# Kernel tuning notes

Measured on AMD Instinct MI355X. Metric: run time of the kernel, lower is better.

Reference implementation:

```python
import jax, jax.numpy as jnp
import numpy as np

H = 1024
B = 8
T = 2048

def setup_inputs() -> dict:
    key = jax.random.key(0)
    ks = jax.random.split(key, 12)
    s = 1.0 / np.sqrt(H)
    return {
        "x": jax.random.normal(ks[0], (B, T, H), dtype=jnp.float32),
        "time_decay": jax.random.normal(ks[1], (H,), dtype=jnp.float32) * 0.1,
        "time_first": jax.random.normal(ks[2], (H,), dtype=jnp.float32) * 0.1,
        "time_mix_key": jax.random.uniform(ks[3], (1, 1, H), dtype=jnp.float32),
        "time_mix_value": jax.random.uniform(ks[4], (1, 1, H), dtype=jnp.float32),
        "time_mix_receptance": jax.random.uniform(ks[5], (1, 1, H), dtype=jnp.float32),
        "Wk": jax.random.normal(ks[6], (H, H), dtype=jnp.float32) * s,
        "Wv": jax.random.normal(ks[7], (H, H), dtype=jnp.float32) * s,
        "Wr": jax.random.normal(ks[8], (H, H), dtype=jnp.float32) * s,
        "Wo": jax.random.normal(ks[9], (H, H), dtype=jnp.float32) * s,
        "bo": jax.random.normal(ks[10], (H,), dtype=jnp.float32) * 0.01,
    }

def reference(x, time_decay, time_first, time_mix_key, time_mix_value,
              time_mix_receptance, Wk, Wv, Wr, Wo, bo):
    # time shift: shifted[:, t] = x[:, t-1], shifted[:, 0] = 0
    shifted = jnp.pad(x, ((0, 0), (1, 0), (0, 0)))[:, :-1]
    k_in = x * time_mix_key + shifted * (1.0 - time_mix_key)
    v_in = x * time_mix_value + shifted * (1.0 - time_mix_value)
    r_in = x * time_mix_receptance + shifted * (1.0 - time_mix_receptance)
    k = jnp.einsum('bth,oh->bto', k_in, Wk)
    v = jnp.einsum('bth,oh->bto', v_in, Wv)
    r = jax.nn.sigmoid(jnp.einsum('bth,oh->bto', r_in, Wr))

    td = jnp.exp(-jnp.exp(time_decay))  # (H,)

    def step(carry, kv):
        num, den = carry            # (B, H) each
        k_t, v_t = kv               # (B, H) each
        e = jnp.exp(time_first + k_t)
        out_t = (num + e * v_t) / (den + e)
        ek = jnp.exp(k_t)
        return (td * num + ek * v_t, td * den + ek), out_t

    init = (jnp.zeros((x.shape[0], x.shape[2]), x.dtype),
            jnp.zeros((x.shape[0], x.shape[2]), x.dtype))
    # scan over time: (T, B, H)
    _, wkv = jax.lax.scan(step, init, (k.transpose(1, 0, 2), v.transpose(1, 0, 2)))
    wkv = wkv.transpose(1, 0, 2)    # (B, T, H)

    return jnp.einsum('bth,oh->bto', r * wkv, Wo) + bo
```

## Files before the change

kernel.cpp:

```cpp
#include <hip/hip_runtime.h>
#include <hip/hip_bf16.h>
#include <cstdint>
#include <cstddef>

#define HH 1024
#define BB 8
#define TT 2048
#define MM (BB*TT)
#define CC 256
#define LL (TT/CC)

typedef __attribute__((ext_vector_type(8))) short bf16x8;
typedef __attribute__((ext_vector_type(8))) unsigned short u16x8;
typedef __attribute__((ext_vector_type(4))) float f32x4;

__device__ __forceinline__ unsigned short f2bf(float f) {
  union { float f; unsigned u; } v; v.f = f;
  return (unsigned short)((v.u + 0x7fffu + ((v.u >> 16) & 1u)) >> 16);
}
__device__ __forceinline__ float bf2f(unsigned short s) {
  union { float f; unsigned u; } v; v.u = ((unsigned)s) << 16;
  return v.f;
}

__device__ __forceinline__ void load_lds16(const void* g, void* l) {
  __builtin_amdgcn_global_load_lds((const __attribute__((address_space(1))) void*)g,
                                   (__attribute__((address_space(3))) void*)l,
                                   16, 0, 0);
}

__global__ __launch_bounds__(256) void conv_w(const float* __restrict__ Wk,
    const float* __restrict__ Wv, const float* __restrict__ Wr,
    const float* __restrict__ Wo, unsigned short* __restrict__ dst) {
  const int i = (blockIdx.x * 256 + threadIdx.x) * 4;
  const float* src = blockIdx.y == 0 ? Wk : blockIdx.y == 1 ? Wv : blockIdx.y == 2 ? Wr : Wo;
  const float4 v = *(const float4*)(src + i);
  ushort4 o; o.x = f2bf(v.x); o.y = f2bf(v.y); o.z = f2bf(v.z); o.w = f2bf(v.w);
  *(ushort4*)(dst + (size_t)blockIdx.y * HH * HH + i) = o;
}

__global__ __launch_bounds__(256) void mix_kernel(const float* __restrict__ x,
    const float* __restrict__ tmk, const float* __restrict__ tmv, const float* __restrict__ tmr,
    unsigned short* __restrict__ kin, unsigned short* __restrict__ vin,
    unsigned short* __restrict__ rin) {
  const int gid = blockIdx.x * 256 + threadIdx.x;
  const size_t e0 = (size_t)gid * 4;
  const int h = (int)(e0 & (HH - 1));
  const int t = (int)((e0 >> 10) & (TT - 1));
  const float4 xv = *(const float4*)(x + e0);
  float4 sv = make_float4(0.f, 0.f, 0.f, 0.f);
  if (t != 0) sv = *(const float4*)(x + e0 - HH);
  const float4 k4 = *(const float4*)(tmk + h);
  const float4 v4 = *(const float4*)(tmv + h);
  const float4 r4 = *(const float4*)(tmr + h);
  ushort4 ko, vo, ro;
  ko.x = f2bf(sv.x + k4.x * (xv.x - sv.x)); ko.y = f2bf(sv.y + k4.y * (xv.y - sv.y));
  ko.z = f2bf(sv.z + k4.z * (xv.z - sv.z)); ko.w = f2bf(sv.w + k4.w * (xv.w - sv.w));
  vo.x = f2bf(sv.x + v4.x * (xv.x - sv.x)); vo.y = f2bf(sv.y + v4.y * (xv.y - sv.y));
  vo.z = f2bf(sv.z + v4.z * (xv.z - sv.z)); vo.w = f2bf(sv.w + v4.w * (xv.w - sv.w));
  ro.x = f2bf(sv.x + r4.x * (xv.x - sv.x)); ro.y = f2bf(sv.y + r4.y * (xv.y - sv.y));
  ro.z = f2bf(sv.z + r4.z * (xv.z - sv.z)); ro.w = f2bf(sv.w + r4.w * (xv.w - sv.w));
  *(ushort4*)(kin + e0) = ko;
  *(ushort4*)(vin + e0) = vo;
  *(ushort4*)(rin + e0) = ro;
}


#define BAR()   do { asm volatile("" ::: "memory"); __builtin_amdgcn_s_barrier(); \
                     asm volatile("" ::: "memory"); } while (0)
#define SB0()   __builtin_amdgcn_sched_barrier(0)
#define VM4()   asm volatile("s_waitcnt vmcnt(4)" ::: "memory")
#define VM0()   asm volatile("s_waitcnt vmcnt(0)" ::: "memory")

__device__ __forceinline__ void stA(const unsigned short* __restrict__ Ag, int m0, int kt,
                                    unsigned short* buf, int h, int w, int rl, int scol) {
#pragma unroll
  for (int l = 0; l < 2; ++l) {
    const int row = l * 128 + h * 64 + w * 8;
    load_lds16(Ag + (size_t)(m0 + row + rl) * HH + kt + scol, buf + row * 64);
  }
}
__device__ __forceinline__ void stB(const unsigned short* __restrict__ Bg, int n0, int kt,
                                    unsigned short* buf, int h, int w, int rl, int scol) {
#pragma unroll
  for (int l = 0; l < 2; ++l) {
    const int row = (2 * (l * 2 + (w >> 2)) + h) * 32 + (w & 3) * 8;
    load_lds16(Bg + (size_t)(n0 + row + rl) * HH + kt + scol, buf + row * 64);
  }
}

template<int MH, int FH>
__device__ __forceinline__ void rdA_h(const unsigned short* buf, bf16x8 (&af)[4][2],
                                      int wm, int l15, int kq, int swz) {
#pragma unroll
  for (int fm = FH * 2; fm < FH * 2 + 2; ++fm)
#pragma unroll
    for (int kk = 0; kk < 2; ++kk)
      af[fm][kk] = *(const bf16x8*)(buf + (wm * 128 + MH * 64 + fm * 16 + l15) * 64
                                        + ((kk * 32 + kq * 8) ^ swz));
}
template<int NH>
__device__ __forceinline__ void rdB(const unsigned short* buf, bf16x8 (&bfr)[2][2][2],
                                    int wn, int l15, int kq, int swz) {
#pragma unroll
  for (int fn = 0; fn < 2; ++fn)
#pragma unroll
    for (int kk = 0; kk < 2; ++kk)
      bfr[NH][fn][kk] = *(const bf16x8*)(buf + (wn * 64 + NH * 32 + fn * 16 + l15) * 64
                                             + ((kk * 32 + kq * 8) ^ swz));
}
template<int MH, int NH, int FH>
__device__ __forceinline__ void mfma8(f32x4 (&acc)[8][4], const bf16x8 (&af)[4][2],
                                      const bf16x8 (&bfr)[2][2][2]) {
#pragma unroll
  for (int kk = 0; kk < 2; ++kk)
#pragma unroll
    for (int fm = FH * 2; fm < FH * 2 + 2; ++fm)
#pragma unroll
      for (int fn = 0; fn < 2; ++fn)
        acc[MH * 4 + fm][NH * 2 + fn] = __builtin_amdgcn_mfma_f32_16x16x32_bf16(
            bfr[NH][fn][kk], af[fm][kk], acc[MH * 4 + fm][NH * 2 + fn], 0, 0, 0);
}

__device__ __forceinline__ void gemm256(const unsigned short* __restrict__ Ag,
                                        const unsigned short* __restrict__ Bg,
                                        const int m0, const int n0,
                                        unsigned short* As, unsigned short* Bs,
                                        f32x4 (&acc)[8][4]) {
  const int tid = threadIdx.x;
  const int lane = tid & 63;
  const int w = tid >> 6;
  const int wm = w >> 2, wn = w & 3;
  const int l15 = lane & 15, kq = lane >> 4;
  const int swz = (l15 & 7) << 3;
  const int rl = lane >> 3;
  const int scol = ((lane & 7) ^ rl) * 8;
  unsigned short* const A0 = As;
  unsigned short* const A1 = As + 256 * 64;
  unsigned short* const B0 = Bs;
  unsigned short* const B1 = Bs + 256 * 64;
  bf16x8 af[4][2], bfr[2][2][2];

  stA(Ag, m0, 0, A0, 0, w, rl, scol);
  stB(Bg, n0, 0, B0, 0, w, rl, scol);
  stB(Bg, n0, 0, B0, 1, w, rl, scol);
  stA(Ag, m0, 0, A0, 1, w, rl, scol);
  stA(Ag, m0, 64, A1, 0, w, rl, scol);
  stB(Bg, n0, 64, B1, 0, w, rl, scol);
  VM4();
  BAR();

#pragma unroll 1
  for (int i = 0; i < 8; ++i) {
    const int t1  = ((2 * i + 1) * 64) & (HH - 1);
    const int tn0 = ((2 * i + 2) * 64) & (HH - 1);
    const int tn1 = ((2 * i + 3) * 64) & (HH - 1);

    rdA_h<0, 0>(A0, af, wm, l15, kq, swz); SB0();
    rdB<0>(B0, bfr, wn, l15, kq, swz);     SB0();
    rdA_h<0, 1>(A0, af, wm, l15, kq, swz); SB0();
    rdB<1>(B0, bfr, wn, l15, kq, swz);
    stB(Bg, n0, t1, B1, 1, w, rl, scol);
    stA(Ag, m0, t1, A1, 1, w, rl, scol);
    BAR(); SB0();
    __builtin_amdgcn_s_setprio(1);
    mfma8<0, 0, 0>(acc, af, bfr); SB0();
    mfma8<0, 0, 1>(acc, af, bfr); SB0();
    mfma8<0, 1, 0>(acc, af, bfr);
    mfma8<0, 1, 1>(acc, af, bfr);
    __builtin_amdgcn_s_setprio(0);
    BAR();
    rdA_h<1, 0>(A0, af, wm, l15, kq, swz); SB0();
    rdA_h<1, 1>(A0, af, wm, l15, kq, swz);
    stA(Ag, m0, tn0, A0, 0, w, rl, scol);
    stB(Bg, n0, tn0, B0, 0, w, rl, scol);
    BAR(); SB0();
    __builtin_amdgcn_s_setprio(1);
    mfma8<1, 0, 0>(acc, af, bfr);
    mfma8<1, 1, 0>(acc, af, bfr); SB0();
    mfma8<1, 0, 1>(acc, af, bfr);
    mfma8<1, 1, 1>(acc, af, bfr);
    __builtin_amdgcn_s_setprio(0);
    VM4();
    BAR();
    rdA_h<0, 0>(A1, af, wm, l15, kq, swz); SB0();
    rdB<0>(B1, bfr, wn, l15, kq, swz);     SB0();
    rdA_h<0, 1>(A1, af, wm, l15, kq, swz); SB0();
    rdB<1>(B1, bfr, wn, l15, kq, swz);
    stB(Bg, n0, tn0, B0, 1, w, rl, scol);
    stA(Ag, m0, tn0, A0, 1, w, rl, scol);
    BAR(); SB0();
    __builtin_amdgcn_s_setprio(1);
    mfma8<0, 0, 0>(acc, af, bfr); SB0();
    mfma8<0, 0, 1>(acc, af, bfr); SB0();
    mfma8<0, 1, 0>(acc, af, bfr);
    mfma8<0, 1, 1>(acc, af, bfr);
    __builtin_amdgcn_s_setprio(0);
    BAR();
    rdA_h<1, 0>(A1, af, wm, l15, kq, swz); SB0();
    rdA_h<1, 1>(A1, af, wm, l15, kq, swz);
    stA(Ag, m0, tn1, A1, 0, w, rl, scol);
    stB(Bg, n0, tn1, B1, 0, w, rl, scol);
    BAR(); SB0();
    __builtin_amdgcn_s_setprio(1);
    mfma8<1, 0, 0>(acc, af, bfr);
    mfma8<1, 1, 0>(acc, af, bfr); SB0();
    mfma8<1, 0, 1>(acc, af, bfr);
    mfma8<1, 1, 1>(acc, af, bfr);
    __builtin_amdgcn_s_setprio(0);
    VM4();
    BAR();
  }
  VM0();
}

__device__ __forceinline__ void swizzle_mn256(int x, int& m0, int& n0) {
  const int wg = (x & 7) * 32 + (x >> 3);
  m0 = (wg >> 2) * 256;
  n0 = (wg & 3) * 256;
}

__global__ __launch_bounds__(512, 2) void gemm_kvr(const unsigned short* __restrict__ kin,
    const unsigned short* __restrict__ vin, const unsigned short* __restrict__ rin,
    const unsigned short* __restrict__ Wbf,
    unsigned short* __restrict__ kb, unsigned short* __restrict__ vb,
    unsigned short* __restrict__ rb) {
  __shared__ unsigned short As[2 * 256 * 64];
  __shared__ unsigned short Bs[2 * 256 * 64];
  const int z = blockIdx.y;
  const unsigned short* Ag = z == 0 ? kin : (z == 1 ? vin : rin);
  const unsigned short* Bg = Wbf + (size_t)z * HH * HH;
  unsigned short* Cg = z == 0 ? kb : (z == 1 ? vb : rb);
  int m0, n0; swizzle_mn256(blockIdx.x, m0, n0);
  f32x4 acc[8][4] = {};
  gemm256(Ag, Bg, m0, n0, As, Bs, acc);
  const int lane = threadIdx.x & 63, w = threadIdx.x >> 6;
  const int wm = w >> 2, wn = w & 3, l15 = lane & 15, lq = lane >> 4;
  const bool sig = (z == 2);
#pragma unroll
  for (int fm = 0; fm < 8; ++fm) {
    const size_t mrow = (size_t)(m0 + wm * 128 + fm * 16 + l15) * HH;
#pragma unroll
    for (int fn = 0; fn < 4; ++fn) {
      const int ncol = n0 + wn * 64 + fn * 16 + lq * 4;
      float v0 = acc[fm][fn][0], v1 = acc[fm][fn][1];
      float v2 = acc[fm][fn][2], v3 = acc[fm][fn][3];
      if (sig) {
        v0 = 1.0f / (1.0f + __expf(-v0)); v1 = 1.0f / (1.0f + __expf(-v1));
        v2 = 1.0f / (1.0f + __expf(-v2)); v3 = 1.0f / (1.0f + __expf(-v3));
      }
      ushort4 o; o.x = f2bf(v0); o.y = f2bf(v1); o.z = f2bf(v2); o.w = f2bf(v3);
      *(ushort4*)(Cg + mrow + ncol) = o;
    }
  }
}

__global__ __launch_bounds__(512, 2) void gemm_o(const unsigned short* __restrict__ Ag,
    const unsigned short* __restrict__ Bg, const float* __restrict__ bias,
    float* __restrict__ C) {
  __shared__ unsigned short As[2 * 256 * 64];
  __shared__ unsigned short Bs[2 * 256 * 64];
  int m0, n0; swizzle_mn256(blockIdx.x, m0, n0);
  f32x4 acc[8][4] = {};
  gemm256(Ag, Bg, m0, n0, As, Bs, acc);
  const int lane = threadIdx.x & 63, w = threadIdx.x >> 6;
  const int wm = w >> 2, wn = w & 3, l15 = lane & 15, lq = lane >> 4;
#pragma unroll
  for (int fm = 0; fm < 8; ++fm) {
    const size_t mrow = (size_t)(m0 + wm * 128 + fm * 16 + l15) * HH;
#pragma unroll
    for (int fn = 0; fn < 4; ++fn) {
      const int ncol = n0 + wn * 64 + fn * 16 + lq * 4;
      const float4 bv = *(const float4*)(bias + ncol);
      float4 ov;
      ov.x = acc[fm][fn][0] + bv.x; ov.y = acc[fm][fn][1] + bv.y;
      ov.z = acc[fm][fn][2] + bv.z; ov.w = acc[fm][fn][3] + bv.w;
      *(float4*)(C + mrow + ncol) = ov;
    }
  }
}

__global__ __launch_bounds__(256) void wkv_part(const unsigned short* __restrict__ k,
    const unsigned short* __restrict__ v, const float* __restrict__ tdec,
    float* __restrict__ pnum, float* __restrict__ pden) {
  const int gid = blockIdx.x * 256 + threadIdx.x;
  const int h0 = (gid & 127) * 8;
  const int b = (gid >> 7) & (BB - 1);
  const int c = gid >> 10;
  float td[8], num[8], den[8];
#pragma unroll
  for (int j = 0; j < 8; ++j) {
    td[j] = __expf(-__expf(tdec[h0 + j]));
    num[j] = 0.f; den[j] = 0.f;
  }
  size_t idx = (size_t)b * TT * HH + (size_t)(c * LL) * HH + h0;
#pragma unroll
  for (int i = 0; i < LL; ++i, idx += HH) {
    const u16x8 k8 = *(const u16x8*)(k + idx);
    const u16x8 v8 = *(const u16x8*)(v + idx);
#pragma unroll
    for (int j = 0; j < 8; ++j) {
      const float ek = __expf(bf2f(k8[j]));
      num[j] = td[j] * num[j] + ek * bf2f(v8[j]);
      den[j] = td[j] * den[j] + ek;
    }
  }
  const size_t o = (size_t)c * (BB * HH) + b * HH + h0;
#pragma unroll
  for (int j = 0; j < 8; ++j) { pnum[o + j] = num[j]; pden[o + j] = den[j]; }
}

__global__ __launch_bounds__(256) void wkv_scan(const float* __restrict__ tdec,
    float* __restrict__ pnum, float* __restrict__ pden) {
  const int bh = blockIdx.x * 256 + threadIdx.x;
  const int h = bh & (HH - 1);
  const float ed = __expf(tdec[h]);
  const float tdL = __expf(-ed * (float)LL);
  float num = 0.f, den = 0.f;
#pragma unroll 8
  for (int c = 0; c < CC; ++c) {
    const size_t o = (size_t)c * (BB * HH) + bh;
    const float tn = pnum[o], td_ = pden[o];
    pnum[o] = num; pden[o] = den;
    num = tdL * num + tn;
    den = tdL * den + td_;
  }
}

__global__ __launch_bounds__(256) void wkv_final(const unsigned short* __restrict__ k,
    const unsigned short* __restrict__ v, const unsigned short* __restrict__ r,
    const float* __restrict__ tdec, const float* __restrict__ tfst,
    const float* __restrict__ pnum, const float* __restrict__ pden,
    unsigned short* __restrict__ rwkv) {
  const int gid = blockIdx.x * 256 + threadIdx.x;
  const int h0 = (gid & 127) * 8;
  const int b = (gid >> 7) & (BB - 1);
  const int c = gid >> 10;
  float td[8], etf[8], num[8], den[8];
  const size_t o = (size_t)c * (BB * HH) + b * HH + h0;
#pragma unroll
  for (int j = 0; j < 8; ++j) {
    td[j] = __expf(-__expf(tdec[h0 + j]));
    etf[j] = __expf(tfst[h0 + j]);
    num[j] = pnum[o + j]; den[j] = pden[o + j];
  }
  size_t idx = (size_t)b * TT * HH + (size_t)(c * LL) * HH + h0;
#pragma unroll
  for (int i = 0; i < LL; ++i, idx += HH) {
    const u16x8 k8 = *(const u16x8*)(k + idx);
    const u16x8 v8 = *(const u16x8*)(v + idx);
    const u16x8 r8 = *(const u16x8*)(r + idx);
    u16x8 o8;
#pragma unroll
    for (int j = 0; j < 8; ++j) {
      const float ek = __expf(bf2f(k8[j]));
      const float vt = bf2f(v8[j]);
      const float rt = bf2f(r8[j]);
      const float e = ek * etf[j];
      const float inv = __builtin_amdgcn_rcpf(den[j] + e);
      const float outv = (num[j] + e * vt) * inv;
      num[j] = td[j] * num[j] + ek * vt;
      den[j] = td[j] * den[j] + ek;
      o8[j] = f2bf(outv * rt);
    }
    *(u16x8*)(rwkv + idx) = o8;
  }
}

extern "C" void kernel_launch(void* const* d_in, const int* in_sizes, int n_in,
                              void* d_out, int out_size, void* d_ws, size_t ws_size,
                              hipStream_t stream) {
  (void)in_sizes; (void)n_in; (void)out_size; (void)ws_size;
  const float* x    = (const float*)d_in[0];
  const float* tdec = (const float*)d_in[1];
  const float* tfst = (const float*)d_in[2];
  const float* tmk  = (const float*)d_in[3];
  const float* tmv  = (const float*)d_in[4];
  const float* tmr  = (const float*)d_in[5];
  const float* Wk   = (const float*)d_in[6];
  const float* Wv   = (const float*)d_in[7];
  const float* Wr   = (const float*)d_in[8];
  const float* Wo   = (const float*)d_in[9];
  const float* bo   = (const float*)d_in[10];
  float* out = (float*)d_out;

  char* ws = (char*)d_ws;
  const size_t MiB = (size_t)1 << 20;
  unsigned short* Wbf = (unsigned short*)(ws);
  unsigned short* kin = (unsigned short*)(ws + 8 * MiB);
  unsigned short* vin = (unsigned short*)(ws + 40 * MiB);
  unsigned short* rin = (unsigned short*)(ws + 72 * MiB);
  unsigned short* rb  = (unsigned short*)(ws + 104 * MiB);
  unsigned short* kb = (unsigned short*)out;
  unsigned short* vb = kb + (size_t)MM * HH;
  unsigned short* rwkv = kin;
  float* pnum = (float*)(ws + 40 * MiB);
  float* pden = (float*)(ws + 48 * MiB);

  hipLaunchKernelGGL(conv_w, dim3(1024, 4), dim3(256), 0, stream, Wk, Wv, Wr, Wo, Wbf);
  hipLaunchKernelGGL(mix_kernel, dim3(16384), dim3(256), 0, stream,
                     x, tmk, tmv, tmr, kin, vin, rin);
  hipLaunchKernelGGL(gemm_kvr, dim3(256, 3), dim3(512), 0, stream,
                     kin, vin, rin, Wbf, kb, vb, rb);
  hipLaunchKernelGGL(wkv_part, dim3(1024), dim3(256), 0, stream,
                     kb, vb, tdec, pnum, pden);
  hipLaunchKernelGGL(wkv_scan, dim3(32), dim3(256), 0, stream,
                     tdec, pnum, pden);
  hipLaunchKernelGGL(wkv_final, dim3(1024), dim3(256), 0, stream,
                     kb, vb, rb, tdec, tfst, pnum, pden, rwkv);
  hipLaunchKernelGGL(gemm_o, dim3(256), dim3(512), 0, stream,
                     rwkv, Wbf + (size_t)3 * HH * HH, bo, out);
}
```

Measured before the change: 374.1 us.

## Restructure GEMM main loop with register double-buffering and halve WKV chunk count

The GEMM inner loop now reads A fragments into two alternating register sets and loads all B fragments at once, so the next half-tile's LDS reads overlap the current MFMA block. Sched barriers are removed and the loop waits for all global loads instead of leaving four in flight. Separately, the WKV scan uses 128 chunks instead of 256, giving longer sequential runs per thread, fewer partial states and half the grid, with reduced unrolling. This trades more register pressure and less parallelism in the WKV kernels for fewer barriers and less partial-state traffic.

Measured after the change: 431.9 us. +15.5%, slower.

```diff
diff --git a/kernel.cpp b/kernel.cpp
--- a/kernel.cpp
+++ b/kernel.cpp
@@ -7,7 +7,7 @@
 #define BB 8
 #define TT 2048
 #define MM (BB*TT)
-#define CC 256
+#define CC 128
 #define LL (TT/CC)
 
 typedef __attribute__((ext_vector_type(8))) short bf16x8;
@@ -68,9 +68,10 @@
 
 #define BAR()   do { asm volatile("" ::: "memory"); __builtin_amdgcn_s_barrier(); \
                      asm volatile("" ::: "memory"); } while (0)
-#define SB0()   __builtin_amdgcn_sched_barrier(0)
 #define VM4()   asm volatile("s_waitcnt vmcnt(4)" ::: "memory")
 #define VM0()   asm volatile("s_waitcnt vmcnt(0)" ::: "memory")
+#define PRIO1() __builtin_amdgcn_s_setprio(1)
+#define PRIO0() __builtin_amdgcn_s_setprio(0)
 
 __device__ __forceinline__ void stA(const unsigned short* __restrict__ Ag, int m0, int kt,
                                     unsigned short* buf, int h, int w, int rl, int scol) {
@@ -89,37 +90,40 @@
   }
 }
 
-template<int MH, int FH>
-__device__ __forceinline__ void rdA_h(const unsigned short* buf, bf16x8 (&af)[4][2],
-                                      int wm, int l15, int kq, int swz) {
-#pragma unroll
-  for (int fm = FH * 2; fm < FH * 2 + 2; ++fm)
+template<int MH>
+__device__ __forceinline__ void rdA(const unsigned short* buf, bf16x8 (&af)[4][2],
+                                    int wm, int l15, int kq, int swz) {
+#pragma unroll
+  for (int fm = 0; fm < 4; ++fm)
 #pragma unroll
     for (int kk = 0; kk < 2; ++kk)
       af[fm][kk] = *(const bf16x8*)(buf + (wm * 128 + MH * 64 + fm * 16 + l15) * 64
                                         + ((kk * 32 + kq * 8) ^ swz));
 }
-template<int NH>
-__device__ __forceinline__ void rdB(const unsigned short* buf, bf16x8 (&bfr)[2][2][2],
-                                    int wn, int l15, int kq, int swz) {
-#pragma unroll
-  for (int fn = 0; fn < 2; ++fn)
-#pragma unroll
-    for (int kk = 0; kk < 2; ++kk)
-      bfr[NH][fn][kk] = *(const bf16x8*)(buf + (wn * 64 + NH * 32 + fn * 16 + l15) * 64
-                                             + ((kk * 32 + kq * 8) ^ swz));
-}
-template<int MH, int NH, int FH>
-__device__ __forceinline__ void mfma8(f32x4 (&acc)[8][4], const bf16x8 (&af)[4][2],
-                                      const bf16x8 (&bfr)[2][2][2]) {
-#pragma unroll
-  for (int kk = 0; kk < 2; ++kk)
-#pragma unroll
-    for (int fm = FH * 2; fm < FH * 2 + 2; ++fm)
-#pragma unroll
-      for (int fn = 0; fn < 2; ++fn)
-        acc[MH * 4 + fm][NH * 2 + fn] = __builtin_amdgcn_mfma_f32_16x16x32_bf16(
-            bfr[NH][fn][kk], af[fm][kk], acc[MH * 4 + fm][NH * 2 + fn], 0, 0, 0);
+__device__ __forceinline__ void rdBall(const unsigned short* buf, bf16x8 (&bfr)[2][2][2],
+                                       int wn, int l15, int kq, int swz) {
+#pragma unroll
+  for (int nh = 0; nh < 2; ++nh)
+#pragma unroll
+    for (int fn = 0; fn < 2; ++fn)
+#pragma unroll
+      for (int kk = 0; kk < 2; ++kk)
+        bfr[nh][fn][kk] = *(const bf16x8*)(buf + (wn * 64 + nh * 32 + fn * 16 + l15) * 64
+                                               + ((kk * 32 + kq * 8) ^ swz));
+}
+template<int MH>
+__device__ __forceinline__ void mfma32(f32x4 (&acc)[8][4], const bf16x8 (&af)[4][2],
+                                       const bf16x8 (&bfr)[2][2][2]) {
+#pragma unroll
+  for (int nh = 0; nh < 2; ++nh)
+#pragma unroll
+    for (int fn = 0; fn < 2; ++fn)
+#pragma unroll
+      for (int kk = 0; kk < 2; ++kk)
+#pragma unroll
+        for (int fm = 0; fm < 4; ++fm)
+          acc[MH * 4 + fm][nh * 2 + fn] = __builtin_amdgcn_mfma_f32_16x16x32_bf16(
+              bfr[nh][fn][kk], af[fm][kk], acc[MH * 4 + fm][nh * 2 + fn], 0, 0, 0);
 }
 
 __device__ __forceinline__ void gemm256(const unsigned short* __restrict__ Ag,
@@ -139,7 +143,7 @@
   unsigned short* const A1 = As + 256 * 64;
   unsigned short* const B0 = Bs;
   unsigned short* const B1 = Bs + 256 * 64;
-  bf16x8 af[4][2], bfr[2][2][2];
+  bf16x8 afA[4][2], afB[4][2], bfr[2][2][2];
 
   stA(Ag, m0, 0, A0, 0, w, rl, scol);
   stB(Bg, n0, 0, B0, 0, w, rl, scol);
@@ -149,6 +153,8 @@
   stB(Bg, n0, 64, B1, 0, w, rl, scol);
   VM4();
   BAR();
+  rdA<0>(A0, afA, wm, l15, kq, swz);
+  rdBall(B0, bfr, wn, l15, kq, swz);
 
 #pragma unroll 1
   for (int i = 0; i < 8; ++i) {
@@ -156,60 +162,33 @@
     const int tn0 = ((2 * i + 2) * 64) & (HH - 1);
     const int tn1 = ((2 * i + 3) * 64) & (HH - 1);
 
-    rdA_h<0, 0>(A0, af, wm, l15, kq, swz); SB0();
-    rdB<0>(B0, bfr, wn, l15, kq, swz);     SB0();
-    rdA_h<0, 1>(A0, af, wm, l15, kq, swz); SB0();
-    rdB<1>(B0, bfr, wn, l15, kq, swz);
+    BAR();
     stB(Bg, n0, t1, B1, 1, w, rl, scol);
     stA(Ag, m0, t1, A1, 1, w, rl, scol);
-    BAR(); SB0();
-    __builtin_amdgcn_s_setprio(1);
-    mfma8<0, 0, 0>(acc, af, bfr); SB0();
-    mfma8<0, 0, 1>(acc, af, bfr); SB0();
-    mfma8<0, 1, 0>(acc, af, bfr);
-    mfma8<0, 1, 1>(acc, af, bfr);
-    __builtin_amdgcn_s_setprio(0);
+    rdA<1>(A0, afB, wm, l15, kq, swz);
+    PRIO1(); mfma32<0>(acc, afA, bfr); PRIO0();
+
+    VM0();
     BAR();
-    rdA_h<1, 0>(A0, af, wm, l15, kq, swz); SB0();
-    rdA_h<1, 1>(A0, af, wm, l15, kq, swz);
     stA(Ag, m0, tn0, A0, 0, w, rl, scol);
     stB(Bg, n0, tn0, B0, 0, w, rl, scol);
-    BAR(); SB0();
-    __builtin_amdgcn_s_setprio(1);
-    mfma8<1, 0, 0>(acc, af, bfr);
-    mfma8<1, 1, 0>(acc, af, bfr); SB0();
-    mfma8<1, 0, 1>(acc, af, bfr);
-    mfma8<1, 1, 1>(acc, af, bfr);
-    __builtin_amdgcn_s_setprio(0);
-    VM4();
+    rdA<0>(A1, afA, wm, l15, kq, swz);
+    PRIO1(); mfma32<1>(acc, afB, bfr); PRIO0();
+    rdBall(B1, bfr, wn, l15, kq, swz);
+
     BAR();
-    rdA_h<0, 0>(A1, af, wm, l15, kq, swz); SB0();
-    rdB<0>(B1, bfr, wn, l15, kq, swz);     SB0();
-    rdA_h<0, 1>(A1, af, wm, l15, kq, swz); SB0();
-    rdB<1>(B1, bfr, wn, l15, kq, swz);
     stB(Bg, n0, tn0, B0, 1, w, rl, scol);
     stA(Ag, m0, tn0, A0, 1, w, rl, scol);
-    BAR(); SB0();
-    __builtin_amdgcn_s_setprio(1);
-    mfma8<0, 0, 0>(acc, af, bfr); SB0();
-    mfma8<0, 0, 1>(acc, af, bfr); SB0();
-    mfma8<0, 1, 0>(acc, af, bfr);
-    mfma8<0, 1, 1>(acc, af, bfr);
-    __builtin_amdgcn_s_setprio(0);
+    rdA<1>(A1, afB, wm, l15, kq, swz);
+    PRIO1(); mfma32<0>(acc, afA, bfr); PRIO0();
+
+    VM0();
     BAR();
-    rdA_h<1, 0>(A1, af, wm, l15, kq, swz); SB0();
-    rdA_h<1, 1>(A1, af, wm, l15, kq, swz);
     stA(Ag, m0, tn1, A1, 0, w, rl, scol);
     stB(Bg, n0, tn1, B1, 0, w, rl, scol);
-    BAR(); SB0();
-    __builtin_amdgcn_s_setprio(1);
-    mfma8<1, 0, 0>(acc, af, bfr);
-    mfma8<1, 1, 0>(acc, af, bfr); SB0();
-    mfma8<1, 0, 1>(acc, af, bfr);
-    mfma8<1, 1, 1>(acc, af, bfr);
-    __builtin_amdgcn_s_setprio(0);
-    VM4();
-    BAR();
+    rdA<0>(A0, afA, wm, l15, kq, swz);
+    PRIO1(); mfma32<1>(acc, afB, bfr); PRIO0();
+    rdBall(B0, bfr, wn, l15, kq, swz);
   }
   VM0();
 }
@@ -294,7 +273,7 @@
     num[j] = 0.f; den[j] = 0.f;
   }
   size_t idx = (size_t)b * TT * HH + (size_t)(c * LL) * HH + h0;
-#pragma unroll
+#pragma unroll 4
   for (int i = 0; i < LL; ++i, idx += HH) {
     const u16x8 k8 = *(const u16x8*)(k + idx);
     const u16x8 v8 = *(const u16x8*)(v + idx);
@@ -345,7 +324,7 @@
     num[j] = pnum[o + j]; den[j] = pden[o + j];
   }
   size_t idx = (size_t)b * TT * HH + (size_t)(c * LL) * HH + h0;
-#pragma unroll
+#pragma unroll 2
   for (int i = 0; i < LL; ++i, idx += HH) {
     const u16x8 k8 = *(const u16x8*)(k + idx);
     const u16x8 v8 = *(const u16x8*)(v + idx);
@@ -395,18 +374,18 @@
   unsigned short* vb = kb + (size_t)MM * HH;
   unsigned short* rwkv = kin;
   float* pnum = (float*)(ws + 40 * MiB);
-  float* pden = (float*)(ws + 48 * MiB);
+  float* pden = (float*)(ws + 44 * MiB);
 
   hipLaunchKernelGGL(conv_w, dim3(1024, 4), dim3(256), 0, stream, Wk, Wv, Wr, Wo, Wbf);
   hipLaunchKernelGGL(mix_kernel, dim3(16384), dim3(256), 0, stream,
                      x, tmk, tmv, tmr, kin, vin, rin);
   hipLaunchKernelGGL(gemm_kvr, dim3(256, 3), dim3(512), 0, stream,
                      kin, vin, rin, Wbf, kb, vb, rb);
-  hipLaunchKernelGGL(wkv_part, dim3(1024), dim3(256), 0, stream,
+  hipLaunchKernelGGL(wkv_part, dim3(512), dim3(256), 0, stream,
                      kb, vb, tdec, pnum, pden);
   hipLaunchKernelGGL(wkv_scan, dim3(32), dim3(256), 0, stream,
                      tdec, pnum, pden);
-  hipLaunchKernelGGL(wkv_final, dim3(1024), dim3(256), 0, stream,
+  hipLaunchKernelGGL(wkv_final, dim3(512), dim3(256), 0, stream,
                      kb, vb, rb, tdec, tfst, pnum, pden, rwkv);
   hipLaunchKernelGGL(gemm_o, dim3(256), dim3(512), 0, stream,
                      rwkv, Wbf + (size_t)3 * HH * HH, bo, out);
```
